# Kernel optimization log

Hardware: AMD Instinct MI355X
Metric: run time of the kernel (lower is better)

The kernel has to match this reference:

```python
import jax, jax.numpy as jnp
import numpy as np

D_MODEL = 1024
NUM_HEADS = 16
D_K = D_MODEL // NUM_HEADS
B, T = 2, 2048


def setup_inputs() -> dict:
    key = jax.random.key(0)
    ks = jax.random.split(key, 9)
    s = 1.0 / np.sqrt(D_MODEL)
    inp = {"x": jax.random.normal(ks[0], (B, T, D_MODEL), dtype=jnp.float32)}
    for i, name in enumerate(["q", "k", "v", "out"]):
        inp[f"W_{name}"] = jax.random.uniform(ks[1 + 2 * i], (D_MODEL, D_MODEL), jnp.float32, -s, s)
        inp[f"b_{name}"] = jax.random.uniform(ks[2 + 2 * i], (D_MODEL,), jnp.float32, -s, s)
    return inp


def reference(x, W_q, b_q, W_k, b_k, W_v, b_v, W_out, b_out):
    b, t, _ = x.shape
    # torch Linear: y = x @ W.T + b
    def proj(inp, W, bias):
        y = inp @ W.T + bias
        return y.reshape(b, -1, NUM_HEADS, D_K).transpose(0, 2, 1, 3)  # [B,H,T,d_k]

    Q = proj(x, W_q, b_q)
    K = proj(x, W_k, b_k)
    V = proj(x, W_v, b_v)
    scores = jnp.einsum("bhqd,bhkd->bhqk", Q, K) / jnp.sqrt(jnp.float32(D_K))
    attn = jax.nn.softmax(scores, axis=-1)
    ctx = jnp.einsum("bhqk,bhkd->bhqd", attn, V)
    ctx = ctx.transpose(0, 2, 1, 3).reshape(b, t, D_MODEL)
    return ctx @ W_out.T + b_out
```

## Files before the change

kernel.cpp:

```cpp
#include <hip/hip_runtime.h>
#include <hip/hip_bf16.h>

typedef __attribute__((ext_vector_type(8))) short short8;
typedef __attribute__((ext_vector_type(4))) short short4v;
typedef __attribute__((ext_vector_type(4))) float floatx4;

__device__ __forceinline__ unsigned short f2b(float f) {
  unsigned int v;
  __builtin_memcpy(&v, &f, 4);
  unsigned int r = (v + 0x7FFFu + ((v >> 16) & 1u)) >> 16;
  return (unsigned short)r;
}

__device__ __forceinline__ unsigned int f2b_pk(float a, float b) {
#if __has_builtin(__builtin_amdgcn_cvt_pk_bf16_f32)
  typedef __attribute__((ext_vector_type(2))) __bf16 bf16x2;
  bf16x2 r = __builtin_amdgcn_cvt_pk_bf16_f32(a, b);
  unsigned int u;
  __builtin_memcpy(&u, &r, 4);
  return u;
#else
  return ((unsigned int)f2b(b) << 16) | (unsigned int)f2b(a);
#endif
}

__device__ __forceinline__ float fast_exp2(float x) {
#if __has_builtin(__builtin_amdgcn_exp2f)
  return __builtin_amdgcn_exp2f(x);
#else
  return __builtin_exp2f(x);
#endif
}

__device__ __forceinline__ void async_copy16(const void* g, void* l) {
  __builtin_amdgcn_global_load_lds(
      (const __attribute__((address_space(1))) unsigned int*)g,
      (__attribute__((address_space(3))) unsigned int*)l, 16, 0, 0);
}

#define QSCALE 0.18033688011112042f


__global__ __launch_bounds__(256) void cvt_all_kernel(
    const float* __restrict__ x,
    const float* __restrict__ w0, const float* __restrict__ w1,
    const float* __restrict__ w2, const float* __restrict__ w3,
    unsigned short* __restrict__ xb,
    unsigned short* __restrict__ d0, unsigned short* __restrict__ d1,
    unsigned short* __restrict__ d2, unsigned short* __restrict__ d3)
{
  int gid = blockIdx.x * 256 + threadIdx.x;
  const float* src;
  unsigned short* dst;
  size_t off;
  if (gid < (1 << 20)) {
    src = x; dst = xb; off = gid;
  } else {
    int g = gid - (1 << 20);
    int w = g >> 18;
    off = g & 0x3FFFF;
    src = (w == 0) ? w0 : (w == 1) ? w1 : (w == 2) ? w2 : w3;
    dst = (w == 0) ? d0 : (w == 1) ? d1 : (w == 2) ? d2 : d3;
  }
  floatx4 v = *(const floatx4*)(src + off * 4);
  unsigned int lo = f2b_pk(v[0], v[1]), hi = f2b_pk(v[2], v[3]);
  unsigned long long r = ((unsigned long long)hi << 32) | lo;
  *(unsigned long long*)(dst + off * 4) = r;
}

__global__ __launch_bounds__(256) void gemm_qkv_kernel(
    const unsigned short* __restrict__ A,
    const unsigned short* __restrict__ W0, const unsigned short* __restrict__ W1,
    const unsigned short* __restrict__ W2,
    const float* __restrict__ bias0, const float* __restrict__ bias1,
    const float* __restrict__ bias2,
    unsigned short* __restrict__ Qo, unsigned short* __restrict__ Ko,
    unsigned short* __restrict__ VTo)
{
  const int z = blockIdx.z;
  const unsigned short* W  = (z == 0) ? W0 : (z == 1) ? W1 : W2;
  const float* bias        = (z == 0) ? bias0 : (z == 1) ? bias1 : bias2;

  __shared__ alignas(16) unsigned short sA[128 * 32];
  __shared__ alignas(16) unsigned short sB[128 * 32];

  const int tid  = threadIdx.x;
  const int lane = tid & 63;
  const int wave = tid >> 6;
  const int col  = lane & 15;
  const int quad = lane >> 4;
  const int wm   = (wave >> 1) * 64;
  const int wn   = (wave & 1) * 64;
  const int m0   = blockIdx.y * 128;
  const int n0   = blockIdx.x * 128;
  const int swz8 = (quad ^ ((col >> 1) & 3)) * 8;

  floatx4 acc[4][4];
#pragma unroll
  for (int i = 0; i < 4; ++i)
#pragma unroll
    for (int j = 0; j < 4; ++j) acc[i][j] = (floatx4){0.f, 0.f, 0.f, 0.f};

  for (int k0 = 0; k0 < 1024; k0 += 32) {
    __syncthreads();
#pragma unroll
    for (int i = 0; i < 2; ++i) {
      int c   = i * 256 + tid;
      int row = c >> 2;
      int cs  = (c & 3) ^ ((c >> 3) & 3);
      int ko  = cs * 8;
      async_copy16(A + (size_t)(m0 + row) * 1024 + k0 + ko, sA + c * 8);
      async_copy16(W + (size_t)(n0 + row) * 1024 + k0 + ko, sB + c * 8);
    }
    __syncthreads();
    short8 af[4], bf[4];
#pragma unroll
    for (int mi = 0; mi < 4; ++mi)
      af[mi] = *(const short8*)(sA + (wm + mi * 16 + col) * 32 + swz8);
#pragma unroll
    for (int ni = 0; ni < 4; ++ni)
      bf[ni] = *(const short8*)(sB + (wn + ni * 16 + col) * 32 + swz8);
#pragma unroll
    for (int mi = 0; mi < 4; ++mi)
#pragma unroll
      for (int ni = 0; ni < 4; ++ni)
        acc[mi][ni] = __builtin_amdgcn_mfma_f32_16x16x32_bf16(af[mi], bf[ni], acc[mi][ni], 0, 0, 0);
  }

#pragma unroll
  for (int ni = 0; ni < 4; ++ni) {
    int n = n0 + wn + ni * 16 + col;
    float bv = bias[n];
#pragma unroll
    for (int mi = 0; mi < 4; ++mi) {
      int mbase = m0 + wm + mi * 16 + quad * 4;
#pragma unroll
      for (int r = 0; r < 4; ++r) {
        int m = mbase + r;
        float val = acc[mi][ni][r] + bv;
        if (z == 0) {
          Qo[(size_t)m * 1024 + n] = f2b(val * QSCALE);
        } else if (z == 1) {
          Ko[(size_t)m * 1024 + n] = f2b(val);
        } else {
          int d = n & 63, h = n >> 6;
          int bb = m >> 11, t = m & 2047;
          VTo[(((size_t)bb * 16 + h) * 64 + d) * 2048 + t] = f2b(val);
        }
      }
    }
  }
}

__global__ __launch_bounds__(256) void gemm_out_kernel(
    const unsigned short* __restrict__ A, const unsigned short* __restrict__ W,
    const float* __restrict__ bias, float* __restrict__ DF)
{
  __shared__ alignas(16) unsigned short sA[128 * 32];
  __shared__ alignas(16) unsigned short sB[64 * 32];

  const int tid  = threadIdx.x;
  const int lane = tid & 63;
  const int wave = tid >> 6;
  const int col  = lane & 15;
  const int quad = lane >> 4;
  const int wm   = (wave >> 1) * 64;
  const int wn   = (wave & 1) * 32;
  const int m0   = blockIdx.y * 128;
  const int n0   = blockIdx.x * 64;
  const int swz8 = (quad ^ ((col >> 1) & 3)) * 8;

  floatx4 acc[4][2];
#pragma unroll
  for (int i = 0; i < 4; ++i)
#pragma unroll
    for (int j = 0; j < 2; ++j) acc[i][j] = (floatx4){0.f, 0.f, 0.f, 0.f};

  for (int k0 = 0; k0 < 1024; k0 += 32) {
    __syncthreads();
#pragma unroll
    for (int i = 0; i < 2; ++i) {
      int c   = i * 256 + tid;
      int row = c >> 2;
      int cs  = (c & 3) ^ ((c >> 3) & 3);
      async_copy16(A + (size_t)(m0 + row) * 1024 + k0 + cs * 8, sA + c * 8);
    }
    {
      int row = tid >> 2;
      int cs  = (tid & 3) ^ ((tid >> 3) & 3);
      async_copy16(W + (size_t)(n0 + row) * 1024 + k0 + cs * 8, sB + tid * 8);
    }
    __syncthreads();
    short8 af[4], bf[2];
#pragma unroll
    for (int mi = 0; mi < 4; ++mi)
      af[mi] = *(const short8*)(sA + (wm + mi * 16 + col) * 32 + swz8);
#pragma unroll
    for (int ni = 0; ni < 2; ++ni)
      bf[ni] = *(const short8*)(sB + (wn + ni * 16 + col) * 32 + swz8);
#pragma unroll
    for (int mi = 0; mi < 4; ++mi)
#pragma unroll
      for (int ni = 0; ni < 2; ++ni)
        acc[mi][ni] = __builtin_amdgcn_mfma_f32_16x16x32_bf16(af[mi], bf[ni], acc[mi][ni], 0, 0, 0);
  }

#pragma unroll
  for (int ni = 0; ni < 2; ++ni) {
    int n = n0 + wn + ni * 16 + col;
    float bv = bias[n];
#pragma unroll
    for (int mi = 0; mi < 4; ++mi) {
      int mbase = m0 + wm + mi * 16 + quad * 4;
#pragma unroll
      for (int r = 0; r < 4; ++r)
        DF[(size_t)(mbase + r) * 1024 + n] = acc[mi][ni][r] + bv;
    }
  }
}

__global__ __launch_bounds__(256, 4) void attention_kernel(
    const unsigned short* __restrict__ Q, const unsigned short* __restrict__ K,
    const unsigned short* __restrict__ VT, unsigned short* __restrict__ CTX)
{
  __shared__ alignas(16) unsigned short sQ[2 * 64 * 32];
  __shared__ alignas(16) unsigned short sK[2 * 64 * 32];
  __shared__ alignas(16) unsigned short sV[2 * 64 * 32];
  __shared__ alignas(16) unsigned short sP[4][16 * 72];

  const int bh = blockIdx.x;
  const int b = bh >> 4, h = bh & 15;
  const int q0 = blockIdx.y * 64;
  const int tid  = threadIdx.x;
  const int lane = tid & 63;
  const int wave = tid >> 6;
  const int col  = lane & 15;
  const int quad = lane >> 4;
  const int swz8 = (quad ^ ((col >> 1) & 3)) * 8;

  const int srow = tid >> 2;
  const int sko  = ((tid & 3) ^ ((tid >> 3) & 3)) * 8;

#pragma unroll
  for (int i = 0; i < 2; ++i) {
    async_copy16(Q + (size_t)(b * 2048 + q0 + srow) * 1024 + h * 64 + i * 32 + sko,
                 sQ + (i * 256 + tid) * 8);
  }
  __syncthreads();
  short8 qf[2];
  qf[0] = *(const short8*)(sQ + (wave * 16 + col) * 32 + swz8);
  qf[1] = *(const short8*)(sQ + 2048 + (wave * 16 + col) * 32 + swz8);

  floatx4 Oacc[4];
#pragma unroll
  for (int f = 0; f < 4; ++f) Oacc[f] = (floatx4){0.f, 0.f, 0.f, 0.f};
  float lacc = 0.f;

  unsigned short* myP = &sP[wave][0];

  for (int kt = 0; kt < 2048; kt += 64) {
    __syncthreads();
#pragma unroll
    for (int i = 0; i < 2; ++i) {
      async_copy16(K + (size_t)(b * 2048 + kt + srow) * 1024 + h * 64 + i * 32 + sko,
                   sK + (i * 256 + tid) * 8);
      async_copy16(VT + ((size_t)bh * 64 + srow) * 2048 + kt + i * 32 + sko,
                   sV + (i * 256 + tid) * 8);
    }
    __syncthreads();

    floatx4 ST[4];
#pragma unroll
    for (int f = 0; f < 4; ++f) {
      ST[f] = (floatx4){0.f, 0.f, 0.f, 0.f};
      short8 kf0 = *(const short8*)(sK + (f * 16 + col) * 32 + swz8);
      ST[f] = __builtin_amdgcn_mfma_f32_16x16x32_bf16(kf0, qf[0], ST[f], 0, 0, 0);
      short8 kf1 = *(const short8*)(sK + 2048 + (f * 16 + col) * 32 + swz8);
      ST[f] = __builtin_amdgcn_mfma_f32_16x16x32_bf16(kf1, qf[1], ST[f], 0, 0, 0);
    }

#pragma unroll
    for (int f = 0; f < 4; ++f) {
      float p0 = fast_exp2(ST[f][0]);
      float p1 = fast_exp2(ST[f][1]);
      float p2 = fast_exp2(ST[f][2]);
      float p3 = fast_exp2(ST[f][3]);
      lacc += (p0 + p1) + (p2 + p3);
      unsigned long long w =
          ((unsigned long long)f2b_pk(p2, p3) << 32) | f2b_pk(p0, p1);
      *(unsigned long long*)(myP + col * 72 + f * 16 + quad * 4) = w;
    }

    short8 pf0 = *(const short8*)(myP + col * 72 + quad * 8);
    short8 pf1 = *(const short8*)(myP + col * 72 + 32 + quad * 8);
#pragma unroll
    for (int f = 0; f < 4; ++f) {
      short8 vf0 = *(const short8*)(sV + (f * 16 + col) * 32 + swz8);
      Oacc[f] = __builtin_amdgcn_mfma_f32_16x16x32_bf16(pf0, vf0, Oacc[f], 0, 0, 0);
      short8 vf1 = *(const short8*)(sV + 2048 + (f * 16 + col) * 32 + swz8);
      Oacc[f] = __builtin_amdgcn_mfma_f32_16x16x32_bf16(pf1, vf1, Oacc[f], 0, 0, 0);
    }
  }

  lacc += __shfl_xor(lacc, 16, 64);
  lacc += __shfl_xor(lacc, 32, 64);
  float inv[4];
#pragma unroll
  for (int r = 0; r < 4; ++r) inv[r] = 1.f / __shfl(lacc, quad * 4 + r, 16);

#pragma unroll
  for (int f = 0; f < 4; ++f) {
#pragma unroll
    for (int r = 0; r < 4; ++r) {
      int q = q0 + wave * 16 + quad * 4 + r;
      int d = f * 16 + col;
      CTX[(size_t)(b * 2048 + q) * 1024 + h * 64 + d] = f2b(Oacc[f][r] * inv[r]);
    }
  }
}

extern "C" void kernel_launch(void* const* d_in, const int* in_sizes, int n_in,
                              void* d_out, int out_size, void* d_ws, size_t ws_size,
                              hipStream_t stream) {
  const float* x   = (const float*)d_in[0];
  const float* W_q = (const float*)d_in[1];
  const float* b_q = (const float*)d_in[2];
  const float* W_k = (const float*)d_in[3];
  const float* b_k = (const float*)d_in[4];
  const float* W_v = (const float*)d_in[5];
  const float* b_v = (const float*)d_in[6];
  const float* W_o = (const float*)d_in[7];
  const float* b_o = (const float*)d_in[8];
  float* out = (float*)d_out;

  const size_t NX = (size_t)4096 * 1024;
  const size_t NW = (size_t)1024 * 1024;

  unsigned short* p   = (unsigned short*)d_ws;
  unsigned short* xb  = p;  p += NX;
  unsigned short* Wqb = p;  p += NW;
  unsigned short* Wkb = p;  p += NW;
  unsigned short* Wvb = p;  p += NW;
  unsigned short* Wob = p;  p += NW;
  unsigned short* Q   = p;  p += NX;
  unsigned short* Kb  = p;  p += NX;
  unsigned short* VT  = p;  p += NX;
  unsigned short* CTX = p;  p += NX;

  dim3 blk(256);
  cvt_all_kernel<<<dim3(8192), blk, 0, stream>>>(
      x, W_q, W_k, W_v, W_o, xb, Wqb, Wkb, Wvb, Wob);
  gemm_qkv_kernel<<<dim3(8, 32, 3), blk, 0, stream>>>(
      xb, Wqb, Wkb, Wvb, b_q, b_k, b_v, Q, Kb, VT);
  attention_kernel<<<dim3(32, 32), blk, 0, stream>>>(Q, Kb, VT, CTX);
  gemm_out_kernel<<<dim3(16, 32), blk, 0, stream>>>(CTX, Wob, b_o, out);
}
```

Baseline: 204.8 us.

## Double-buffer K in attention and deepen GEMM K-tiles to 64

In attention, K tiles are double-buffered: the next K tile is prefetched while the current one is used, and the V load moves to the top of the iteration with a barrier before P·V. Q fragments are now loaded straight from global memory instead of going through shared memory. Both GEMMs now use 64-wide K tiles with an 8-way XOR swizzle, which halves the number of barrier pairs per output tile. The transposed V store is packed into a 64-bit write. The costs are more shared memory per block and a barrier that may still wait on the K prefetch, which would limit the overlap.

Result: no change. 208.3 us (+1.7%).

```diff
diff --git a/kernel.cpp b/kernel.cpp
--- a/kernel.cpp
+++ b/kernel.cpp
@@ -39,7 +39,6 @@
 }
 
 #define QSCALE 0.18033688011112042f
-
 
 __global__ __launch_bounds__(256) void cvt_all_kernel(
     const float* __restrict__ x,
@@ -81,8 +80,8 @@
   const unsigned short* W  = (z == 0) ? W0 : (z == 1) ? W1 : W2;
   const float* bias        = (z == 0) ? bias0 : (z == 1) ? bias1 : bias2;
 
-  __shared__ alignas(16) unsigned short sA[128 * 32];
-  __shared__ alignas(16) unsigned short sB[128 * 32];
+  __shared__ alignas(16) unsigned short sA[128 * 64];
+  __shared__ alignas(16) unsigned short sB[128 * 64];
 
   const int tid  = threadIdx.x;
   const int lane = tid & 63;
@@ -93,7 +92,7 @@
   const int wn   = (wave & 1) * 64;
   const int m0   = blockIdx.y * 128;
   const int n0   = blockIdx.x * 128;
-  const int swz8 = (quad ^ ((col >> 1) & 3)) * 8;
+  const int c7   = col & 7;
 
   floatx4 acc[4][4];
 #pragma unroll
@@ -101,30 +100,33 @@
 #pragma unroll
     for (int j = 0; j < 4; ++j) acc[i][j] = (floatx4){0.f, 0.f, 0.f, 0.f};
 
-  for (int k0 = 0; k0 < 1024; k0 += 32) {
-    __syncthreads();
-#pragma unroll
-    for (int i = 0; i < 2; ++i) {
+  for (int k0 = 0; k0 < 1024; k0 += 64) {
+    __syncthreads();
+#pragma unroll
+    for (int i = 0; i < 4; ++i) {
       int c   = i * 256 + tid;
-      int row = c >> 2;
-      int cs  = (c & 3) ^ ((c >> 3) & 3);
-      int ko  = cs * 8;
+      int row = c >> 3;
+      int ko  = ((c & 7) ^ (row & 7)) * 8;
       async_copy16(A + (size_t)(m0 + row) * 1024 + k0 + ko, sA + c * 8);
       async_copy16(W + (size_t)(n0 + row) * 1024 + k0 + ko, sB + c * 8);
     }
     __syncthreads();
-    short8 af[4], bf[4];
-#pragma unroll
-    for (int mi = 0; mi < 4; ++mi)
-      af[mi] = *(const short8*)(sA + (wm + mi * 16 + col) * 32 + swz8);
-#pragma unroll
-    for (int ni = 0; ni < 4; ++ni)
-      bf[ni] = *(const short8*)(sB + (wn + ni * 16 + col) * 32 + swz8);
-#pragma unroll
-    for (int mi = 0; mi < 4; ++mi)
+#pragma unroll
+    for (int ks = 0; ks < 2; ++ks) {
+      const int rp = ((ks * 4 + quad) ^ c7) * 8;
+      short8 af[4], bf[4];
+#pragma unroll
+      for (int mi = 0; mi < 4; ++mi)
+        af[mi] = *(const short8*)(sA + (wm + mi * 16 + col) * 64 + rp);
 #pragma unroll
       for (int ni = 0; ni < 4; ++ni)
-        acc[mi][ni] = __builtin_amdgcn_mfma_f32_16x16x32_bf16(af[mi], bf[ni], acc[mi][ni], 0, 0, 0);
+        bf[ni] = *(const short8*)(sB + (wn + ni * 16 + col) * 64 + rp);
+#pragma unroll
+      for (int mi = 0; mi < 4; ++mi)
+#pragma unroll
+        for (int ni = 0; ni < 4; ++ni)
+          acc[mi][ni] = __builtin_amdgcn_mfma_f32_16x16x32_bf16(af[mi], bf[ni], acc[mi][ni], 0, 0, 0);
+    }
   }
 
 #pragma unroll
@@ -134,18 +136,20 @@
 #pragma unroll
     for (int mi = 0; mi < 4; ++mi) {
       int mbase = m0 + wm + mi * 16 + quad * 4;
-#pragma unroll
-      for (int r = 0; r < 4; ++r) {
-        int m = mbase + r;
-        float val = acc[mi][ni][r] + bv;
-        if (z == 0) {
-          Qo[(size_t)m * 1024 + n] = f2b(val * QSCALE);
-        } else if (z == 1) {
-          Ko[(size_t)m * 1024 + n] = f2b(val);
-        } else {
-          int d = n & 63, h = n >> 6;
-          int bb = m >> 11, t = m & 2047;
-          VTo[(((size_t)bb * 16 + h) * 64 + d) * 2048 + t] = f2b(val);
+      if (z == 2) {
+        int d = n & 63, h = n >> 6;
+        int bb = mbase >> 11, t = mbase & 2047;
+        unsigned int lo = f2b_pk(acc[mi][ni][0] + bv, acc[mi][ni][1] + bv);
+        unsigned int hi = f2b_pk(acc[mi][ni][2] + bv, acc[mi][ni][3] + bv);
+        unsigned long long wv = ((unsigned long long)hi << 32) | lo;
+        *(unsigned long long*)(VTo + (((size_t)bb * 16 + h) * 64 + d) * 2048 + t) = wv;
+      } else {
+#pragma unroll
+        for (int r = 0; r < 4; ++r) {
+          int m = mbase + r;
+          float val = acc[mi][ni][r] + bv;
+          if (z == 0) Qo[(size_t)m * 1024 + n] = f2b(val * QSCALE);
+          else        Ko[(size_t)m * 1024 + n] = f2b(val);
         }
       }
     }
@@ -156,8 +160,8 @@
     const unsigned short* __restrict__ A, const unsigned short* __restrict__ W,
     const float* __restrict__ bias, float* __restrict__ DF)
 {
-  __shared__ alignas(16) unsigned short sA[128 * 32];
-  __shared__ alignas(16) unsigned short sB[64 * 32];
+  __shared__ alignas(16) unsigned short sA[128 * 64];
+  __shared__ alignas(16) unsigned short sB[64 * 64];
 
   const int tid  = threadIdx.x;
   const int lane = tid & 63;
@@ -168,7 +172,7 @@
   const int wn   = (wave & 1) * 32;
   const int m0   = blockIdx.y * 128;
   const int n0   = blockIdx.x * 64;
-  const int swz8 = (quad ^ ((col >> 1) & 3)) * 8;
+  const int c7   = col & 7;
 
   floatx4 acc[4][2];
 #pragma unroll
@@ -176,33 +180,39 @@
 #pragma unroll
     for (int j = 0; j < 2; ++j) acc[i][j] = (floatx4){0.f, 0.f, 0.f, 0.f};
 
-  for (int k0 = 0; k0 < 1024; k0 += 32) {
-    __syncthreads();
+  for (int k0 = 0; k0 < 1024; k0 += 64) {
+    __syncthreads();
+#pragma unroll
+    for (int i = 0; i < 4; ++i) {
+      int c   = i * 256 + tid;
+      int row = c >> 3;
+      int ko  = ((c & 7) ^ (row & 7)) * 8;
+      async_copy16(A + (size_t)(m0 + row) * 1024 + k0 + ko, sA + c * 8);
+    }
 #pragma unroll
     for (int i = 0; i < 2; ++i) {
       int c   = i * 256 + tid;
-      int row = c >> 2;
-      int cs  = (c & 3) ^ ((c >> 3) & 3);
-      async_copy16(A + (size_t)(m0 + row) * 1024 + k0 + cs * 8, sA + c * 8);
-    }
-    {
-      int row = tid >> 2;
-      int cs  = (tid & 3) ^ ((tid >> 3) & 3);
-      async_copy16(W + (size_t)(n0 + row) * 1024 + k0 + cs * 8, sB + tid * 8);
-    }
-    __syncthreads();
-    short8 af[4], bf[2];
-#pragma unroll
-    for (int mi = 0; mi < 4; ++mi)
-      af[mi] = *(const short8*)(sA + (wm + mi * 16 + col) * 32 + swz8);
-#pragma unroll
-    for (int ni = 0; ni < 2; ++ni)
-      bf[ni] = *(const short8*)(sB + (wn + ni * 16 + col) * 32 + swz8);
-#pragma unroll
-    for (int mi = 0; mi < 4; ++mi)
+      int row = c >> 3;
+      int ko  = ((c & 7) ^ (row & 7)) * 8;
+      async_copy16(W + (size_t)(n0 + row) * 1024 + k0 + ko, sB + c * 8);
+    }
+    __syncthreads();
+#pragma unroll
+    for (int ks = 0; ks < 2; ++ks) {
+      const int rp = ((ks * 4 + quad) ^ c7) * 8;
+      short8 af[4], bf[2];
+#pragma unroll
+      for (int mi = 0; mi < 4; ++mi)
+        af[mi] = *(const short8*)(sA + (wm + mi * 16 + col) * 64 + rp);
 #pragma unroll
       for (int ni = 0; ni < 2; ++ni)
-        acc[mi][ni] = __builtin_amdgcn_mfma_f32_16x16x32_bf16(af[mi], bf[ni], acc[mi][ni], 0, 0, 0);
+        bf[ni] = *(const short8*)(sB + (wn + ni * 16 + col) * 64 + rp);
+#pragma unroll
+      for (int mi = 0; mi < 4; ++mi)
+#pragma unroll
+        for (int ni = 0; ni < 2; ++ni)
+          acc[mi][ni] = __builtin_amdgcn_mfma_f32_16x16x32_bf16(af[mi], bf[ni], acc[mi][ni], 0, 0, 0);
+    }
   }
 
 #pragma unroll
@@ -223,9 +233,8 @@
     const unsigned short* __restrict__ Q, const unsigned short* __restrict__ K,
     const unsigned short* __restrict__ VT, unsigned short* __restrict__ CTX)
 {
-  __shared__ alignas(16) unsigned short sQ[2 * 64 * 32];
-  __shared__ alignas(16) unsigned short sK[2 * 64 * 32];
-  __shared__ alignas(16) unsigned short sV[2 * 64 * 32];
+  __shared__ alignas(16) unsigned short sK[2][4096];
+  __shared__ alignas(16) unsigned short sV[4096];
   __shared__ alignas(16) unsigned short sP[4][16 * 72];
 
   const int bh = blockIdx.x;
@@ -241,15 +250,20 @@
   const int srow = tid >> 2;
   const int sko  = ((tid & 3) ^ ((tid >> 3) & 3)) * 8;
 
-#pragma unroll
-  for (int i = 0; i < 2; ++i) {
-    async_copy16(Q + (size_t)(b * 2048 + q0 + srow) * 1024 + h * 64 + i * 32 + sko,
-                 sQ + (i * 256 + tid) * 8);
-  }
-  __syncthreads();
+  const unsigned short* kbase = K + ((size_t)b * 2048 + srow) * 1024 + h * 64;
+  const unsigned short* vbase = VT + ((size_t)bh * 64 + srow) * 2048;
+
   short8 qf[2];
-  qf[0] = *(const short8*)(sQ + (wave * 16 + col) * 32 + swz8);
-  qf[1] = *(const short8*)(sQ + 2048 + (wave * 16 + col) * 32 + swz8);
+  {
+    const unsigned short* qp =
+        Q + ((size_t)(b * 2048 + q0 + wave * 16 + col)) * 1024 + h * 64 + quad * 8;
+    qf[0] = *(const short8*)qp;
+    qf[1] = *(const short8*)(qp + 32);
+  }
+
+#pragma unroll
+  for (int i = 0; i < 2; ++i)
+    async_copy16(kbase + i * 32 + sko, sK[0] + (i * 256 + tid) * 8);
 
   floatx4 Oacc[4];
 #pragma unroll
@@ -258,24 +272,28 @@
 
   unsigned short* myP = &sP[wave][0];
 
+#pragma unroll 2
   for (int kt = 0; kt < 2048; kt += 64) {
-    __syncthreads();
-#pragma unroll
-    for (int i = 0; i < 2; ++i) {
-      async_copy16(K + (size_t)(b * 2048 + kt + srow) * 1024 + h * 64 + i * 32 + sko,
-                   sK + (i * 256 + tid) * 8);
-      async_copy16(VT + ((size_t)bh * 64 + srow) * 2048 + kt + i * 32 + sko,
-                   sV + (i * 256 + tid) * 8);
-    }
-    __syncthreads();
+    const int cur = (kt >> 6) & 1;
+    const unsigned short* sKc = sK[cur];
+    __syncthreads();
+#pragma unroll
+    for (int i = 0; i < 2; ++i)
+      async_copy16(vbase + kt + i * 32 + sko, sV + (i * 256 + tid) * 8);
+    if (kt + 64 < 2048) {
+#pragma unroll
+      for (int i = 0; i < 2; ++i)
+        async_copy16(kbase + (size_t)(kt + 64) * 1024 + i * 32 + sko,
+                     sK[cur ^ 1] + (i * 256 + tid) * 8);
+    }
 
     floatx4 ST[4];
 #pragma unroll
     for (int f = 0; f < 4; ++f) {
       ST[f] = (floatx4){0.f, 0.f, 0.f, 0.f};
-      short8 kf0 = *(const short8*)(sK + (f * 16 + col) * 32 + swz8);
+      short8 kf0 = *(const short8*)(sKc + (f * 16 + col) * 32 + swz8);
       ST[f] = __builtin_amdgcn_mfma_f32_16x16x32_bf16(kf0, qf[0], ST[f], 0, 0, 0);
-      short8 kf1 = *(const short8*)(sK + 2048 + (f * 16 + col) * 32 + swz8);
+      short8 kf1 = *(const short8*)(sKc + 2048 + (f * 16 + col) * 32 + swz8);
       ST[f] = __builtin_amdgcn_mfma_f32_16x16x32_bf16(kf1, qf[1], ST[f], 0, 0, 0);
     }
 
@@ -290,6 +308,8 @@
           ((unsigned long long)f2b_pk(p2, p3) << 32) | f2b_pk(p0, p1);
       *(unsigned long long*)(myP + col * 72 + f * 16 + quad * 4) = w;
     }
+
+    __syncthreads();
 
     short8 pf0 = *(const short8*)(myP + col * 72 + quad * 8);
     short8 pf1 = *(const short8*)(myP + col * 72 + 32 + quad * 8);
```
